# Optimization experiments

Measured on AMD Instinct MI355X. Metric: run time of the kernel, lower is better.

## Reference

```python
import jax, jax.numpy as jnp
import numpy as np

# Grid / point-count constants (K-Radar-style sparse voxel grid)
B, Z, Y, X = 4, 40, 1024, 1024
Nr, Nl = 262144, 1048576
W_OCC, W_OFF, W_FEAT = 0.2, 1.0, 1.0
BIG = jnp.int32(1_000_000_000)  # sentinel for unmatched candidates


def _hash_zyx(b, z, y, x):
    # max value B*Z*Y*X ~ 1.7e8, fits int32
    return ((b * Z + z) * Y + y) * X + x


def _make_offsets(R):
    rng = np.arange(-R, R + 1)
    dz, dy, dx = np.meshgrid(rng, rng, rng, indexing='ij')
    return jnp.asarray(np.stack([dz.ravel(), dy.ravel(), dx.ravel()], axis=1), dtype=jnp.int32)  # [K,3]


def setup_inputs() -> dict:
    key = jax.random.key(0)
    k = jax.random.split(key, 10)
    radar_indices = jnp.stack([
        jax.random.randint(k[0], (Nr,), 0, B, dtype=jnp.int32),
        jax.random.randint(k[1], (Nr,), 0, Z, dtype=jnp.int32),
        jax.random.randint(k[2], (Nr,), 0, Y, dtype=jnp.int32),
        jax.random.randint(k[3], (Nr,), 0, X, dtype=jnp.int32)], axis=1)
    lidar_indices = jnp.stack([
        jax.random.randint(k[4], (Nl,), 0, B, dtype=jnp.int32),
        jax.random.randint(k[5], (Nl,), 0, Z, dtype=jnp.int32),
        jax.random.randint(k[6], (Nl,), 0, Y, dtype=jnp.int32),
        jax.random.randint(k[7], (Nl,), 0, X, dtype=jnp.int32)], axis=1)
    pred_feat = jax.random.normal(k[8], (Nr, 4), dtype=jnp.float32)
    pred_occ = jax.random.normal(k[9], (Nr, 1, 1), dtype=jnp.float32)
    lidar_features = jax.random.normal(jax.random.fold_in(key, 77), (Nl, 4), dtype=jnp.float32)
    return {"pred_feat": pred_feat, "pred_occ": pred_occ, "radar_indices": radar_indices,
            "lidar_features": lidar_features, "lidar_indices": lidar_indices, "R": 1}


def _local_match(radar_indices, lidar_indices, lidar_features, R):
    # Build sorted hash table of lidar voxels
    hL = _hash_zyx(lidar_indices[:, 0], lidar_indices[:, 1], lidar_indices[:, 2], lidar_indices[:, 3])
    ordL = jnp.argsort(hL)
    hL_sorted = hL[ordL]

    offs = _make_offsets(R)                      # [K,3]
    K = offs.shape[0]
    b, z, y, x = radar_indices[:, 0], radar_indices[:, 1], radar_indices[:, 2], radar_indices[:, 3]
    zz = jnp.clip(z[:, None] + offs[None, :, 0], 0, Z - 1)   # [Nr,K]
    yy = jnp.clip(y[:, None] + offs[None, :, 1], 0, Y - 1)
    xx = jnp.clip(x[:, None] + offs[None, :, 2], 0, X - 1)
    cand = _hash_zyx(b[:, None], zz, yy, xx).reshape(-1)      # [Nr*K]

    pos = jnp.searchsorted(hL_sorted, cand)                   # [Nr*K]
    safe_pos = jnp.clip(pos, 0, hL_sorted.shape[0] - 1)
    is_member = (pos < hL_sorted.shape[0]) & (hL_sorted[safe_pos] == cand)
    hit = is_member.reshape(-1, K)                            # [Nr,K]

    dL1 = jnp.sum(jnp.abs(offs), axis=1)                      # [K]
    dL1_masked = jnp.where(hit, dL1[None, :], BIG)            # [Nr,K]
    best_k = jnp.argmin(dL1_masked, axis=1)                   # [Nr]
    best = jnp.take_along_axis(dL1_masked, best_k[:, None], axis=1)[:, 0]
    matched = best < BIG                                      # [Nr] bool

    pos_flat = jnp.take_along_axis(pos.reshape(-1, K), best_k[:, None], axis=1)[:, 0]
    lidar_row = ordL[jnp.clip(pos_flat, 0, hL_sorted.shape[0] - 1)]
    gt_feat = jnp.where(matched[:, None], lidar_features[lidar_row], 0.0)  # [Nr, C_lidar]

    sel_z = jnp.take_along_axis(zz, best_k[:, None], axis=1)[:, 0]
    sel_y = jnp.take_along_axis(yy, best_k[:, None], axis=1)[:, 0]
    sel_x = jnp.take_along_axis(xx, best_k[:, None], axis=1)[:, 0]
    gt_offsets = jnp.stack([sel_z - z, sel_y - y, sel_x - x], axis=1).astype(jnp.float32)
    return matched, gt_offsets, gt_feat


def reference(pred_feat, pred_occ, radar_indices, lidar_features, lidar_indices, R):
    matched, gt_d, gt_f = _local_match(radar_indices, lidar_indices, lidar_features, R)
    gt_d = gt_d[:, ::-1]                              # torch.flip(gt_d, dims=[1])
    m = matched.astype(pred_feat.dtype)

    # BCEWithLogitsLoss(mean): logaddexp(0,x) - x*y
    occ_logits = jnp.mean(jnp.squeeze(pred_occ, axis=1), axis=-1)  # [Nr]
    occ_loss = jnp.mean(jnp.logaddexp(0.0, occ_logits) - occ_logits * m)

    cnt = jnp.sum(m)
    # smooth_l1 (beta=1, mean) over matched rows of pred offsets [M,3]
    diff = pred_feat[:, :3] - gt_d
    ad = jnp.abs(diff)
    sl1 = jnp.where(ad < 1.0, 0.5 * diff * diff, ad - 0.5)
    off_loss = jnp.sum(sl1 * m[:, None]) / jnp.maximum(cnt * 3.0, 1.0)
    # l1 (mean) over matched intensity column [M,1]
    feat_loss = jnp.sum(jnp.abs(pred_feat[:, 3:4] - gt_f[:, 3:4]) * m[:, None]) / jnp.maximum(cnt, 1.0)

    return W_OCC * occ_loss + W_OFF * off_loss + W_FEAT * feat_loss
```

## Files before the change

### kernel.cpp

```cpp
#include <hip/hip_runtime.h>
#include <math.h>
#include <limits.h>

#define BD 4
#define ZD 40
#define YD 1024
#define XD 1024
#define BZYX 167772160

constexpr int BLOCK = 256;
constexpr unsigned SMALL_LOG = 18;
constexpr unsigned SMASK = (1u << SMALL_LOG) - 1;
constexpr size_t BM_BYTES   = (size_t)BZYX / 8;
constexpr size_t STAB_BYTES = (size_t)8 << SMALL_LOG;

__device__ __forceinline__ unsigned hash_mix(unsigned x) {
    x ^= x >> 16; x *= 0x7feb352dU;
    x ^= x >> 15; x *= 0x846ca68bU;
    x ^= x >> 16;
    return x;
}
__device__ __forceinline__ float smooth_l1(float d) {
    float ad = fabsf(d);
    return (ad < 1.0f) ? 0.5f * d * d : ad - 0.5f;
}
__device__ __forceinline__ float logaddexp0(float l) {
    return (l > 0.0f) ? (l + log1pf(expf(-l))) : log1pf(expf(l));
}

__device__ __forceinline__ unsigned cell_gid(int b, int z, int y, int x) {
    unsigned line = ((unsigned)(b * (ZD >> 3) + (z >> 3)) * (YD >> 3) + (y >> 3)) * (XD >> 3) + (x >> 3);
    unsigned bit  = ((unsigned)(z & 7) << 6) | ((unsigned)(y & 7) << 3) | (unsigned)(x & 7);
    return (line << 9) | bit;
}
__device__ __forceinline__ bool bm_test(const unsigned* __restrict__ bm, unsigned gid) {
    return (bm[gid >> 5] >> (gid & 31)) & 1u;
}

__device__ __forceinline__ bool match27(const unsigned* __restrict__ bm,
                                        int b, int z, int y, int x,
                                        int& sz, int& sy, int& sx) {
    const int zc0 = max(z - 1, 0), zc2 = min(z + 1, ZD - 1);
    const int yc0 = max(y - 1, 0), yc2 = min(y + 1, YD - 1);
    const int xc0 = max(x - 1, 0), xc2 = min(x + 1, XD - 1);
    const int zc[3] = {zc0, z, zc2};
    const int yc[3] = {yc0, y, yc2};
    const int xc[3] = {xc0, x, xc2};
    unsigned hm = 0;
#pragma unroll
    for (int a = 0; a < 3; ++a)
#pragma unroll
        for (int c = 0; c < 3; ++c)
#pragma unroll
            for (int d = 0; d < 3; ++d)
                hm |= ((unsigned)bm_test(bm, cell_gid(b, zc[a], yc[c], xc[d]))) << (a * 9 + c * 3 + d);
    constexpr unsigned M0 = 1u << 13;
    constexpr unsigned M1 = (1u << 4) | (1u << 10) | (1u << 12) | (1u << 14) | (1u << 16) | (1u << 22);
    constexpr unsigned M2 = (1u << 1) | (1u << 3) | (1u << 5) | (1u << 7) | (1u << 9) | (1u << 11) |
                            (1u << 15) | (1u << 17) | (1u << 19) | (1u << 21) | (1u << 23) | (1u << 25);
    int bk;
    if (hm & M0)      bk = 13;
    else if (hm & M1) bk = __ffs((int)(hm & M1)) - 1;
    else if (hm & M2) bk = __ffs((int)(hm & M2)) - 1;
    else if (hm)      bk = __ffs((int)hm) - 1;
    else return false;
    const int ai = bk / 9, ci = (bk / 3) % 3, di = bk % 3;
    sz = (ai == 0) ? zc0 : ((ai == 1) ? z : zc2);
    sy = (ci == 0) ? yc0 : ((ci == 1) ? y : yc2);
    sx = (di == 0) ? xc0 : ((di == 1) ? x : xc2);
    return true;
}

__device__ bool matchR(const unsigned* __restrict__ bm, int R,
                       int b, int z, int y, int x, int& sz, int& sy, int& sx) {
    int bestd = INT_MAX; bool m = false;
    for (int dz = -R; dz <= R; ++dz) {
        const int zz = min(max(z + dz, 0), ZD - 1);
        const int adz = abs(dz);
        for (int dy = -R; dy <= R; ++dy) {
            const int yy = min(max(y + dy, 0), YD - 1);
            const int adzy = adz + abs(dy);
            for (int dx = -R; dx <= R; ++dx) {
                const int d = adzy + abs(dx);
                if (d >= bestd) continue;
                const int xx = min(max(x + dx, 0), XD - 1);
                if (bm_test(bm, cell_gid(b, zz, yy, xx))) {
                    bestd = d; m = true; sz = zz; sy = yy; sx = xx;
                }
            }
        }
    }
    return m;
}

__device__ __forceinline__ void stab_insert(unsigned long long* stab, unsigned gid) {
    const unsigned long long desired = ((unsigned long long)(gid + 1) << 32);
    unsigned s = hash_mix(gid) & SMASK;
    while (true) {
        unsigned long long old = atomicCAS(&stab[s], 0ull, desired);
        if (old == 0ull || (unsigned)(old >> 32) == gid + 1) return;
        s = (s + 1) & SMASK;
    }
}
__device__ __forceinline__ void stab_minrow(unsigned long long* stab, unsigned gid, unsigned row) {
    unsigned s = hash_mix(gid) & SMASK;
    while (true) {
        const unsigned long long e = stab[s];
        if (e == 0ull) return;
        if ((unsigned)(e >> 32) == gid + 1) {
            atomicMax((unsigned*)&stab[s], ~row);
            return;
        }
        s = (s + 1) & SMASK;
    }
}
__device__ __forceinline__ unsigned stab_getrow(const unsigned long long* stab, unsigned gid) {
    unsigned s = hash_mix(gid) & SMASK;
    while (true) {
        const unsigned long long e = stab[s];
        if ((unsigned)(e >> 32) == gid + 1) return ~((unsigned)e);
        s = (s + 1) & SMASK;
    }
}

__global__ void k_clear(uint2* __restrict__ wsv, int n2) {
    const uint2 z = make_uint2(0u, 0u);
    const int stride = gridDim.x * blockDim.x;
    for (int k = blockIdx.x * blockDim.x + threadIdx.x; k < n2; k += stride)
        wsv[k] = z;
}

__global__ void k_build(const int4* __restrict__ li, int Nl,
                        unsigned* __restrict__ bm, unsigned* __restrict__ cells) {
    const int j = blockIdx.x * blockDim.x + threadIdx.x;
    if (j >= Nl) return;
    int4 v = li[j];
    const unsigned gid = cell_gid(v.x, v.y, v.z, v.w);
    cells[j] = gid;
    atomicOr(&bm[gid >> 5], 1u << (gid & 31));
}

__global__ void __launch_bounds__(BLOCK)
k_match(const float4* __restrict__ pf, const float* __restrict__ occ,
        const int4* __restrict__ ri, const unsigned* __restrict__ bm,
        unsigned long long* __restrict__ stab, const int* __restrict__ Rptr,
        int Nr, int* __restrict__ mcell, double* __restrict__ partials) {
    const int R = *Rptr;
    double occ_s = 0.0, cnt_s = 0.0, off_s = 0.0;
    const int stride = gridDim.x * blockDim.x;
    for (int i = blockIdx.x * BLOCK + threadIdx.x; i < Nr; i += stride) {
        int4 rib = ri[i];
        const int b = rib.x, z = rib.y, y = rib.z, x = rib.w;
        int sz = 0, sy = 0, sx = 0;
        const bool matched = (R == 1) ? match27(bm, b, z, y, x, sz, sy, sx)
                                      : matchR(bm, R, b, z, y, x, sz, sy, sx);
        float m = 0.f; int mc = -1;
        if (matched) {
            m = 1.f; cnt_s += 1.0;
            const float4 pp = pf[i];
            off_s += (double)(smooth_l1(pp.x - (float)(sx - x)) +
                              smooth_l1(pp.y - (float)(sy - y)) +
                              smooth_l1(pp.z - (float)(sz - z)));
            const unsigned gid = cell_gid(b, sz, sy, sx);
            stab_insert(stab, gid);
            mc = (int)gid;
        }
        mcell[i] = mc;
        const float lg = occ[i];
        occ_s += (double)(logaddexp0(lg) - lg * m);
    }
    __shared__ double sh[3][BLOCK];
    const int tid = threadIdx.x;
    sh[0][tid] = occ_s; sh[1][tid] = cnt_s; sh[2][tid] = off_s;
    __syncthreads();
    for (int s = BLOCK / 2; s > 0; s >>= 1) {
        if (tid < s) {
            sh[0][tid] += sh[0][tid + s];
            sh[1][tid] += sh[1][tid + s];
            sh[2][tid] += sh[2][tid + s];
        }
        __syncthreads();
    }
    if (tid == 0) {
        partials[blockIdx.x * 4 + 0] = sh[0][0];
        partials[blockIdx.x * 4 + 1] = sh[1][0];
        partials[blockIdx.x * 4 + 2] = sh[2][0];
        partials[blockIdx.x * 4 + 3] = 0.0;
    }
}

__global__ void k_scan(const unsigned* __restrict__ cells, int Nl,
                       unsigned long long* __restrict__ stab) {
    const int j = blockIdx.x * blockDim.x + threadIdx.x;
    if (j >= Nl) return;
    stab_minrow(stab, cells[j], (unsigned)j);
}

__global__ void __launch_bounds__(BLOCK)
k_feat(const float* __restrict__ pfw, const int* __restrict__ mcell,
       const unsigned long long* __restrict__ stab, const float* __restrict__ lf,
       int Nr, double* __restrict__ fpart, const double* __restrict__ partials,
       unsigned* __restrict__ counter, int mblk, float* __restrict__ out) {
    double fs = 0.0;
    const int stride = gridDim.x * blockDim.x;
    for (int i = blockIdx.x * BLOCK + threadIdx.x; i < Nr; i += stride) {
        const int mc = mcell[i];
        if (mc >= 0) {
            const unsigned row = stab_getrow(stab, (unsigned)mc);
            fs += (double)fabsf(pfw[(size_t)i * 4 + 3] - lf[(size_t)row * 4 + 3]);
        }
    }
    __shared__ double sh[4][BLOCK];
    __shared__ bool isLast;
    const int tid = threadIdx.x;
    sh[0][tid] = fs;
    __syncthreads();
    for (int s = BLOCK / 2; s > 0; s >>= 1) {
        if (tid < s) sh[0][tid] += sh[0][tid + s];
        __syncthreads();
    }
    if (tid == 0) {
        fpart[blockIdx.x] = sh[0][0];
        __threadfence();
        const unsigned done = atomicAdd(counter, 1u);
        isLast = (done == gridDim.x - 1);
    }
    __syncthreads();
    if (!isLast) return;

    double a0 = 0, a1 = 0, a2 = 0, a3 = 0;
    for (int k = tid; k < mblk; k += BLOCK) {
        a0 += partials[k * 4 + 0];
        a1 += partials[k * 4 + 1];
        a2 += partials[k * 4 + 2];
    }
    for (int k = tid; k < (int)gridDim.x; k += BLOCK) a3 += fpart[k];
    __syncthreads();
    sh[0][tid] = a0; sh[1][tid] = a1; sh[2][tid] = a2; sh[3][tid] = a3;
    __syncthreads();
    for (int s = BLOCK / 2; s > 0; s >>= 1) {
        if (tid < s) {
            sh[0][tid] += sh[0][tid + s];
            sh[1][tid] += sh[1][tid + s];
            sh[2][tid] += sh[2][tid + s];
            sh[3][tid] += sh[3][tid + s];
        }
        __syncthreads();
    }
    if (tid == 0) {
        const double occ_loss = sh[0][0] / (double)Nr;
        const double cnt = sh[1][0];
        const double off_loss = sh[2][0] / fmax(cnt * 3.0, 1.0);
        const double feat_loss = sh[3][0] / fmax(cnt, 1.0);
        out[0] = (float)(0.2 * occ_loss + 1.0 * off_loss + 1.0 * feat_loss);
    }
}

extern "C" void kernel_launch(void* const* d_in, const int* in_sizes, int n_in,
                              void* d_out, int out_size, void* d_ws, size_t ws_size,
                              hipStream_t stream) {
    const float4* pf = (const float4*)d_in[0];
    const float*  oc = (const float*)d_in[1];
    const int4*   ri = (const int4*)d_in[2];
    const float*  lf = (const float*)d_in[3];
    const int4*   li = (const int4*)d_in[4];
    const int*    Rp = (const int*)d_in[5];

    const int Nr = in_sizes[0] / 4;
    const int Nl = in_sizes[3] / 4;
    const int nblkL = (Nl + BLOCK - 1) / BLOCK;
    int nblk = (Nr + BLOCK - 1) / BLOCK;
    if (nblk > 2048) nblk = 2048;

    size_t off = 0;
    auto alloc = [&](size_t n) { size_t o = off; off += (n + 255) & ~(size_t)255; return o; };
    char* ws = (char*)d_ws;
    unsigned*           bm    = (unsigned*)(ws + alloc(BM_BYTES));
    unsigned long long* stab  = (unsigned long long*)(ws + alloc(STAB_BYTES));
    unsigned*           counter = (unsigned*)(ws + alloc(256));
    const size_t zeroBytes = off;
    unsigned*           cells = (unsigned*)(ws + alloc((size_t)Nl * 4));
    int*                mcell = (int*)(ws + alloc((size_t)Nr * 4));
    double*             parts = (double*)(ws + alloc((size_t)nblk * 4 * sizeof(double)));
    double*             fpart = (double*)(ws + alloc((size_t)nblk * sizeof(double)));

    k_clear<<<2048, BLOCK, 0, stream>>>((uint2*)ws, (int)(zeroBytes / 8));
    k_build<<<nblkL, BLOCK, 0, stream>>>(li, Nl, bm, cells);
    k_match<<<nblk, BLOCK, 0, stream>>>(pf, oc, ri, bm, stab, Rp, Nr, mcell, parts);
    k_scan<<<nblkL, BLOCK, 0, stream>>>(cells, Nl, stab);
    k_feat<<<nblk, BLOCK, 0, stream>>>((const float*)pf, mcell, stab, lf, Nr, fpart,
                                       parts, counter, nblk, (float*)d_out);
}
```

Before: 127.9 us.

## Use flat bitmap layout with row-wise 64-bit window probes and slot indices

```diff
diff --git a/kernel.cpp b/kernel.cpp
--- a/kernel.cpp
+++ b/kernel.cpp
@@ -14,6 +14,8 @@
 constexpr size_t BM_BYTES   = (size_t)BZYX / 8;
 constexpr size_t STAB_BYTES = (size_t)8 << SMALL_LOG;
 
+typedef unsigned uvec4 __attribute__((ext_vector_type(4)));
+
 __device__ __forceinline__ unsigned hash_mix(unsigned x) {
     x ^= x >> 16; x *= 0x7feb352dU;
     x ^= x >> 15; x *= 0x846ca68bU;
@@ -28,32 +30,38 @@
     return (l > 0.0f) ? (l + log1pf(expf(-l))) : log1pf(expf(l));
 }
 
-__device__ __forceinline__ unsigned cell_gid(int b, int z, int y, int x) {
-    unsigned line = ((unsigned)(b * (ZD >> 3) + (z >> 3)) * (YD >> 3) + (y >> 3)) * (XD >> 3) + (x >> 3);
-    unsigned bit  = ((unsigned)(z & 7) << 6) | ((unsigned)(y & 7) << 3) | (unsigned)(x & 7);
-    return (line << 9) | bit;
-}
-__device__ __forceinline__ bool bm_test(const unsigned* __restrict__ bm, unsigned gid) {
-    return (bm[gid >> 5] >> (gid & 31)) & 1u;
+__device__ __forceinline__ unsigned cell_flat(int b, int z, int y, int x) {
+    return ((unsigned)(b * ZD + z) * YD + y) * XD + (unsigned)x;
+}
+__device__ __forceinline__ bool bm_test(const unsigned* __restrict__ bm, unsigned c) {
+    return (bm[c >> 5] >> (c & 31)) & 1u;
 }
 
 __device__ __forceinline__ bool match27(const unsigned* __restrict__ bm,
                                         int b, int z, int y, int x,
                                         int& sz, int& sy, int& sx) {
-    const int zc0 = max(z - 1, 0), zc2 = min(z + 1, ZD - 1);
-    const int yc0 = max(y - 1, 0), yc2 = min(y + 1, YD - 1);
-    const int xc0 = max(x - 1, 0), xc2 = min(x + 1, XD - 1);
-    const int zc[3] = {zc0, z, zc2};
-    const int yc[3] = {yc0, y, yc2};
-    const int xc[3] = {xc0, x, xc2};
+    const int xa = max(x - 1, 0);
+    const int xc = min(x + 1, XD - 1);
+    const int sa = x - xa;
+    const int sc = xc - xa;
     unsigned hm = 0;
 #pragma unroll
-    for (int a = 0; a < 3; ++a)
+    for (int dz = -1; dz <= 1; ++dz) {
+        const int zz = min(max(z + dz, 0), ZD - 1);
 #pragma unroll
-        for (int c = 0; c < 3; ++c)
-#pragma unroll
-            for (int d = 0; d < 3; ++d)
-                hm |= ((unsigned)bm_test(bm, cell_gid(b, zc[a], yc[c], xc[d]))) << (a * 9 + c * 3 + d);
+        for (int dy = -1; dy <= 1; ++dy) {
+            const int yy = min(max(y + dy, 0), YD - 1);
+            const unsigned n0 = cell_flat(b, zz, yy, xa);
+            const unsigned q = n0 >> 5;
+            const int r = n0 & 31;
+            unsigned long long w = ((unsigned long long)bm[q + 1] << 32) | bm[q];
+            w >>= r;
+            const int k0 = (dz + 1) * 9 + (dy + 1) * 3;
+            hm |= ((unsigned)(w & 1)) << (k0 + 0);
+            hm |= ((unsigned)((w >> sa) & 1)) << (k0 + 1);
+            hm |= ((unsigned)((w >> sc) & 1)) << (k0 + 2);
+        }
+    }
     constexpr unsigned M0 = 1u << 13;
     constexpr unsigned M1 = (1u << 4) | (1u << 10) | (1u << 12) | (1u << 14) | (1u << 16) | (1u << 22);
     constexpr unsigned M2 = (1u << 1) | (1u << 3) | (1u << 5) | (1u << 7) | (1u << 9) | (1u << 11) |
@@ -65,9 +73,9 @@
     else if (hm)      bk = __ffs((int)hm) - 1;
     else return false;
     const int ai = bk / 9, ci = (bk / 3) % 3, di = bk % 3;
-    sz = (ai == 0) ? zc0 : ((ai == 1) ? z : zc2);
-    sy = (ci == 0) ? yc0 : ((ci == 1) ? y : yc2);
-    sx = (di == 0) ? xc0 : ((di == 1) ? x : xc2);
+    sz = min(max(z + ai - 1, 0), ZD - 1);
+    sy = min(max(y + ci - 1, 0), YD - 1);
+    sx = (di == 0) ? xa : ((di == 1) ? x : xc);
     return true;
 }
 
@@ -84,7 +92,7 @@
                 const int d = adzy + abs(dx);
                 if (d >= bestd) continue;
                 const int xx = min(max(x + dx, 0), XD - 1);
-                if (bm_test(bm, cell_gid(b, zz, yy, xx))) {
+                if (bm_test(bm, cell_flat(b, zz, yy, xx))) {
                     bestd = d; m = true; sz = zz; sy = yy; sx = xx;
                 }
             }
@@ -93,41 +101,33 @@
     return m;
 }
 
-__device__ __forceinline__ void stab_insert(unsigned long long* stab, unsigned gid) {
-    const unsigned long long desired = ((unsigned long long)(gid + 1) << 32);
-    unsigned s = hash_mix(gid) & SMASK;
+__device__ __forceinline__ unsigned stab_insert(unsigned long long* stab, unsigned key) {
+    const unsigned long long desired = ((unsigned long long)key << 32);
+    unsigned s = hash_mix(key) & SMASK;
     while (true) {
         unsigned long long old = atomicCAS(&stab[s], 0ull, desired);
-        if (old == 0ull || (unsigned)(old >> 32) == gid + 1) return;
+        if (old == 0ull || (unsigned)(old >> 32) == key) return s;
         s = (s + 1) & SMASK;
     }
 }
-__device__ __forceinline__ void stab_minrow(unsigned long long* stab, unsigned gid, unsigned row) {
-    unsigned s = hash_mix(gid) & SMASK;
+__device__ __forceinline__ void stab_minrow(unsigned long long* stab, unsigned key, unsigned row) {
+    unsigned s = hash_mix(key) & SMASK;
     while (true) {
         const unsigned long long e = stab[s];
         if (e == 0ull) return;
-        if ((unsigned)(e >> 32) == gid + 1) {
+        if ((unsigned)(e >> 32) == key) {
             atomicMax((unsigned*)&stab[s], ~row);
             return;
         }
         s = (s + 1) & SMASK;
     }
 }
-__device__ __forceinline__ unsigned stab_getrow(const unsigned long long* stab, unsigned gid) {
-    unsigned s = hash_mix(gid) & SMASK;
-    while (true) {
-        const unsigned long long e = stab[s];
-        if ((unsigned)(e >> 32) == gid + 1) return ~((unsigned)e);
-        s = (s + 1) & SMASK;
-    }
-}
-
-__global__ void k_clear(uint2* __restrict__ wsv, int n2) {
-    const uint2 z = make_uint2(0u, 0u);
+
+__global__ void k_clear(uvec4* __restrict__ v, int n4) {
+    const uvec4 z = (uvec4)(0u);
     const int stride = gridDim.x * blockDim.x;
-    for (int k = blockIdx.x * blockDim.x + threadIdx.x; k < n2; k += stride)
-        wsv[k] = z;
+    for (int k = blockIdx.x * blockDim.x + threadIdx.x; k < n4; k += stride)
+        __builtin_nontemporal_store(z, &v[k]);
 }
 
 __global__ void k_build(const int4* __restrict__ li, int Nl,
@@ -135,9 +135,9 @@
     const int j = blockIdx.x * blockDim.x + threadIdx.x;
     if (j >= Nl) return;
     int4 v = li[j];
-    const unsigned gid = cell_gid(v.x, v.y, v.z, v.w);
-    cells[j] = gid;
-    atomicOr(&bm[gid >> 5], 1u << (gid & 31));
+    const unsigned c = cell_flat(v.x, v.y, v.z, v.w);
+    cells[j] = c;
+    atomicOr(&bm[c >> 5], 1u << (c & 31));
 }
 
 __global__ void __launch_bounds__(BLOCK)
@@ -154,18 +154,17 @@
         int sz = 0, sy = 0, sx = 0;
         const bool matched = (R == 1) ? match27(bm, b, z, y, x, sz, sy, sx)
                                       : matchR(bm, R, b, z, y, x, sz, sy, sx);
-        float m = 0.f; int mc = -1;
+        float m = 0.f; int ms = -1;
         if (matched) {
             m = 1.f; cnt_s += 1.0;
             const float4 pp = pf[i];
             off_s += (double)(smooth_l1(pp.x - (float)(sx - x)) +
                               smooth_l1(pp.y - (float)(sy - y)) +
                               smooth_l1(pp.z - (float)(sz - z)));
-            const unsigned gid = cell_gid(b, sz, sy, sx);
-            stab_insert(stab, gid);
-            mc = (int)gid;
-        }
-        mcell[i] = mc;
+            const unsigned c = cell_flat(b, sz, sy, sx);
+            ms = (int)stab_insert(stab, c + 1);
+        }
+        mcell[i] = ms;
         const float lg = occ[i];
         occ_s += (double)(logaddexp0(lg) - lg * m);
     }
@@ -193,7 +192,7 @@
                        unsigned long long* __restrict__ stab) {
     const int j = blockIdx.x * blockDim.x + threadIdx.x;
     if (j >= Nl) return;
-    stab_minrow(stab, cells[j], (unsigned)j);
+    stab_minrow(stab, cells[j] + 1, (unsigned)j);
 }
 
 __global__ void __launch_bounds__(BLOCK)
@@ -204,9 +203,9 @@
     double fs = 0.0;
     const int stride = gridDim.x * blockDim.x;
     for (int i = blockIdx.x * BLOCK + threadIdx.x; i < Nr; i += stride) {
-        const int mc = mcell[i];
-        if (mc >= 0) {
-            const unsigned row = stab_getrow(stab, (unsigned)mc);
+        const int ms = mcell[i];
+        if (ms >= 0) {
+            const unsigned row = ~((unsigned)stab[ms]);
             fs += (double)fabsf(pfw[(size_t)i * 4 + 3] - lf[(size_t)row * 4 + 3]);
         }
     }
@@ -275,16 +274,16 @@
     size_t off = 0;
     auto alloc = [&](size_t n) { size_t o = off; off += (n + 255) & ~(size_t)255; return o; };
     char* ws = (char*)d_ws;
-    unsigned*           bm    = (unsigned*)(ws + alloc(BM_BYTES));
-    unsigned long long* stab  = (unsigned long long*)(ws + alloc(STAB_BYTES));
+    unsigned*           bm      = (unsigned*)(ws + alloc(BM_BYTES + 256));
+    unsigned long long* stab    = (unsigned long long*)(ws + alloc(STAB_BYTES));
     unsigned*           counter = (unsigned*)(ws + alloc(256));
-    const size_t zeroBytes = off;
+    const size_t zeroEnd = off;
     unsigned*           cells = (unsigned*)(ws + alloc((size_t)Nl * 4));
     int*                mcell = (int*)(ws + alloc((size_t)Nr * 4));
     double*             parts = (double*)(ws + alloc((size_t)nblk * 4 * sizeof(double)));
     double*             fpart = (double*)(ws + alloc((size_t)nblk * sizeof(double)));
 
-    k_clear<<<2048, BLOCK, 0, stream>>>((uint2*)ws, (int)(zeroBytes / 8));
+    k_clear<<<4096, BLOCK, 0, stream>>>((uvec4*)ws, (int)(zeroEnd / 16));
     k_build<<<nblkL, BLOCK, 0, stream>>>(li, Nl, bm, cells);
     k_match<<<nblk, BLOCK, 0, stream>>>(pf, oc, ri, bm, stab, Rp, Nr, mcell, parts);
     k_scan<<<nblkL, BLOCK, 0, stream>>>(cells, Nl, stab);
```

After: 138.0 us. 1.08x slower.
